# Performance work log

Measured on AMD Instinct MI355X. Metric: run time of the kernel, lower is better.

Reference implementation:

```python
import jax, jax.numpy as jnp
import numpy as np

N_NODES = 50000
N_EDGES = 600000
F_IN = 57
HID = 128
NEG_SLOPE = 0.2  # PyG GATConv default leaky_relu slope


def setup_inputs() -> dict:
    key = jax.random.key(0)
    ks = jax.random.split(key, 10)
    s = lambda k, shape, fan: jax.random.normal(k, shape, jnp.float32) / np.float32(np.sqrt(fan))
    x = jax.random.normal(ks[0], (N_NODES, F_IN), jnp.float32)
    edge_index = jax.random.randint(ks[1], (2, N_EDGES), 0, N_NODES)
    return {
        "x": x,
        "edge_index": edge_index,
        # layer1: GATConv(57 -> 128, heads=1)
        "W_gat": s(ks[2], (F_IN, HID), F_IN),
        "a_src": s(ks[3], (HID,), HID),
        "a_dst": s(ks[4], (HID,), HID),
        "b_gat": jnp.zeros((HID,), jnp.float32),
        # layer2: SAGEConv(128 -> 128, aggr='mean'): lin_l (with bias) on aggregated, lin_r (no bias) on self
        "W_l": s(ks[5], (HID, HID), HID),
        "b_l": jnp.zeros((HID,), jnp.float32),
        "W_r": s(ks[6], (HID, HID), HID),
        # layer3: Linear(128 -> 1)
        "W_out": s(ks[7], (HID, 1), HID),
        "b_out": jnp.zeros((1,), jnp.float32),
    }


def _gat_conv(x, src, dst, W, a_s, a_d, b, n):
    # PyG GATConv (heads=1): adds self-loops, attention softmax over incoming edges per dst node.
    loop = jnp.arange(n)
    src = jnp.concatenate([src, loop])
    dst = jnp.concatenate([dst, loop])
    h = x @ W                                   # [N, H]
    logit = jax.nn.leaky_relu((h @ a_s)[src] + (h @ a_d)[dst], NEG_SLOPE)  # [E+N]
    lmax = jax.lax.stop_gradient(jax.ops.segment_max(logit, dst, num_segments=n))
    ex = jnp.exp(logit - lmax[dst])
    denom = jax.ops.segment_sum(ex, dst, num_segments=n)
    alpha = ex / denom[dst]
    out = jax.ops.segment_sum(alpha[:, None] * h[src], dst, num_segments=n)  # [N, H]
    return out + b


def _sage_conv_mean(x, src, dst, W_l, b_l, W_r, n):
    # PyG SAGEConv: out = lin_l(mean_{j->i} x_j) + lin_r(x_i); no self-loops.
    msum = jax.ops.segment_sum(x[src], dst, num_segments=n)          # [N, H]
    cnt = jax.ops.segment_sum(jnp.ones_like(src, jnp.float32), dst, num_segments=n)
    mean = msum / jnp.maximum(cnt, 1.0)[:, None]
    return mean @ W_l + b_l + x @ W_r


def reference(x, edge_index, W_gat, a_src, a_dst, b_gat, W_l, b_l, W_r, W_out, b_out):
    n = x.shape[0]
    src, dst = edge_index[0], edge_index[1]
    h = jax.nn.relu(_gat_conv(x, src, dst, W_gat, a_src, a_dst, b_gat, n))
    h = jax.nn.relu(_sage_conv_mean(h, src, dst, W_l, b_l, W_r, n))
    return jax.nn.sigmoid(h @ W_out + b_out)  # [N, 1]
```

## Files before the change

kernel.cpp:

```cpp
#include <hip/hip_runtime.h>

#define NN 50000
#define NE 600000
#define F_IN 57
#define HID 128
#define NEG 0.2f
#define NB_SCAN ((NN + 255) / 256)

#define GIN_NODES 64
#define NB_GIN ((NN + GIN_NODES - 1) / GIN_NODES)
#define XST 68

#define DN_NODES 64
#define NB_DENSE ((NN + DN_NODES - 1) / DN_NODES)

typedef unsigned short bf16_t;
typedef __attribute__((ext_vector_type(8))) short bf16x8;
typedef __attribute__((ext_vector_type(4))) float f32x4;

__device__ __forceinline__ float leaky(float v) { return v >= 0.f ? v : NEG * v; }
__device__ __forceinline__ float bf2f(bf16_t u) { return __uint_as_float(((unsigned)u) << 16); }
__device__ __forceinline__ bf16_t f2bf(float f) {
    unsigned u = __float_as_uint(f);
    return (bf16_t)((u + 0x7FFFu + ((u >> 16) & 1u)) >> 16);
}

__global__ __launch_bounds__(256) void k_gat_in(
    const float* __restrict__ x, const float* __restrict__ Wg,
    const float* __restrict__ a_s, const float* __restrict__ a_d,
    bf16_t* __restrict__ h, float* __restrict__ hs, float* __restrict__ hd) {
    __shared__ float WgS[F_IN * HID];
    __shared__ float xsT[F_IN][XST];
    int tid = threadIdx.x;
    int node0 = blockIdx.x * GIN_NODES;
    {
        const float4* g = (const float4*)Wg;
        float4* s = (float4*)WgS;
        for (int i = tid; i < F_IN * HID / 4; i += 256) s[i] = g[i];
    }
    for (int i = tid; i < GIN_NODES * F_IN; i += 256) {
        int n = i / F_IN;
        int k = i - n * F_IN;
        int gn = node0 + n;
        if (gn >= NN) gn = NN - 1;
        xsT[k][n] = x[gn * F_IN + k];
    }
    __syncthreads();

    int fq = tid & 31, nq = tid >> 5;
    int f0 = fq * 4, nb = nq * 8;
    float acc[8][4];
#pragma unroll
    for (int i = 0; i < 8; ++i)
#pragma unroll
        for (int j = 0; j < 4; ++j) acc[i][j] = 0.f;

    for (int k = 0; k < F_IN; ++k) {
        float4 w = *(const float4*)&WgS[k * HID + f0];
        float4 xa = *(const float4*)&xsT[k][nb];
        float4 xb = *(const float4*)&xsT[k][nb + 4];
        float xv[8] = {xa.x, xa.y, xa.z, xa.w, xb.x, xb.y, xb.z, xb.w};
        float wv[4] = {w.x, w.y, w.z, w.w};
#pragma unroll
        for (int i = 0; i < 8; ++i)
#pragma unroll
            for (int j = 0; j < 4; ++j)
                acc[i][j] = fmaf(xv[i], wv[j], acc[i][j]);
    }

    float4 as4 = *(const float4*)(a_s + f0);
    float4 ad4 = *(const float4*)(a_d + f0);
    float ps[8], pd[8];
#pragma unroll
    for (int i = 0; i < 8; ++i) {
        int gn = node0 + nb + i;
        if (gn < NN) {
            ushort4 hv;
            hv.x = f2bf(acc[i][0]); hv.y = f2bf(acc[i][1]);
            hv.z = f2bf(acc[i][2]); hv.w = f2bf(acc[i][3]);
            *(ushort4*)(h + (size_t)gn * HID + f0) = hv;
        }
        ps[i] = acc[i][0] * as4.x + acc[i][1] * as4.y + acc[i][2] * as4.z + acc[i][3] * as4.w;
        pd[i] = acc[i][0] * ad4.x + acc[i][1] * ad4.y + acc[i][2] * ad4.z + acc[i][3] * ad4.w;
    }
#pragma unroll
    for (int off = 16; off > 0; off >>= 1) {
#pragma unroll
        for (int i = 0; i < 8; ++i) {
            ps[i] += __shfl_xor(ps[i], off);
            pd[i] += __shfl_xor(pd[i], off);
        }
    }
    if (fq == 0) {
#pragma unroll
        for (int i = 0; i < 8; ++i) {
            int gn = node0 + nb + i;
            if (gn < NN) { hs[gn] = ps[i]; hd[gn] = pd[i]; }
        }
    }
}

__global__ __launch_bounds__(256) void k_pack_w(
    const float* __restrict__ Wl, const float* __restrict__ Wr, bf16_t* __restrict__ Bp) {
    int idx = blockIdx.x * 256 + threadIdx.x;
    if (idx >= 8 * 8 * 64) return;
    int lane = idx & 63;
    int kb = (idx >> 6) & 7;
    int nt = idx >> 9;
    int col = nt * 16 + (lane & 15);
    int kbase = kb * 32 + (lane >> 4) * 8;
    bf16_t v[8];
#pragma unroll
    for (int j = 0; j < 8; ++j) {
        int k = kbase + j;
        float w = (k < HID) ? Wl[k * HID + col] : Wr[(k - HID) * HID + col];
        v[j] = f2bf(w);
    }
    ushort4* o = (ushort4*)(Bp + (size_t)idx * 8);
    ushort4 lo, hi;
    lo.x = v[0]; lo.y = v[1]; lo.z = v[2]; lo.w = v[3];
    hi.x = v[4]; hi.y = v[5]; hi.z = v[6]; hi.w = v[7];
    o[0] = lo; o[1] = hi;
}

__global__ void k_hist(const int* __restrict__ dst, int* __restrict__ deg) {
    int e = blockIdx.x * blockDim.x + threadIdx.x;
    if (e < NE) atomicAdd(&deg[dst[e]], 1);
}

__global__ void k_scan1(const int* __restrict__ deg, int* __restrict__ rptr, int* __restrict__ bsum) {
    int t = threadIdx.x;
    int i = blockIdx.x * 256 + t;
    int v = (i < NN) ? deg[i] : 0;
    __shared__ int s[256];
    s[t] = v;
    __syncthreads();
    for (int off = 1; off < 256; off <<= 1) {
        int x = (t >= off) ? s[t - off] : 0;
        __syncthreads();
        s[t] += x;
        __syncthreads();
    }
    if (i < NN) rptr[i] = s[t] - v;
    if (t == 255) bsum[blockIdx.x] = s[255];
}

__global__ void k_scan3(int* __restrict__ rptr, const int* __restrict__ bsum) {
    int t = threadIdx.x;
    int v = (t < NB_SCAN && t < blockIdx.x) ? bsum[t] : 0;
#pragma unroll
    for (int off = 32; off > 0; off >>= 1) v += __shfl_xor(v, off);
    __shared__ int wsum[4];
    if ((t & 63) == 0) wsum[t >> 6] = v;
    __syncthreads();
    int pre = wsum[0] + wsum[1] + wsum[2] + wsum[3];
    int i = blockIdx.x * 256 + t;
    if (i < NN) rptr[i] += pre;
}

__global__ void k_fill(const int* __restrict__ src, const int* __restrict__ dst,
                       const int* __restrict__ rptr, int* __restrict__ fill,
                       int* __restrict__ esrc) {
    int e = blockIdx.x * blockDim.x + threadIdx.x;
    if (e >= NE) return;
    int d = dst[e];
    int pos = rptr[d] + atomicAdd(&fill[d], 1);
    esrc[pos] = src[e];
}

__global__ __launch_bounds__(256) void k_gat_agg(
    const int* __restrict__ rptr, const int* __restrict__ deg,
    const int* __restrict__ esrc, const float* __restrict__ hs,
    const float* __restrict__ hd, const bf16_t* __restrict__ h,
    const float* __restrict__ bg, bf16_t* __restrict__ h1) {
    int tid = threadIdx.x;
    int row = blockIdx.x * 4 + (tid >> 6);
    if (row >= NN) return;
    int lane = tid & 63;
    int slot = lane >> 4;
    int f8 = lane & 15;

    int start = rptr[row];
    int dn = deg[row];
    int end = start + dn;
    float hdr = hd[row];
    float wself = __expf(leaky(hs[row] + hdr));

    float a[8];
#pragma unroll
    for (int j = 0; j < 8; ++j) a[j] = 0.f;
    float denL = 0.f;

    if (slot == 0) {
        bf16x8 r = *(const bf16x8*)(h + (size_t)row * HID + f8 * 8);
#pragma unroll
        for (int j = 0; j < 8; ++j) a[j] = wself * bf2f((bf16_t)r[j]);
    }

    int e = start;
    for (; e + 8 <= end; e += 8) {
        int s0 = esrc[e + slot];
        int s1 = esrc[e + 4 + slot];
        float w0 = __expf(leaky(hs[s0] + hdr));
        float w1 = __expf(leaky(hs[s1] + hdr));
        bf16x8 r0 = *(const bf16x8*)(h + (size_t)s0 * HID + f8 * 8);
        bf16x8 r1 = *(const bf16x8*)(h + (size_t)s1 * HID + f8 * 8);
        denL += w0 + w1;
#pragma unroll
        for (int j = 0; j < 8; ++j) {
            a[j] = fmaf(w0, bf2f((bf16_t)r0[j]), a[j]);
            a[j] = fmaf(w1, bf2f((bf16_t)r1[j]), a[j]);
        }
    }
    for (; e < end; e += 4) {
        int i = e + slot;
        bool act = i < end;
        int sn = esrc[act ? i : end - 1];
        float w = act ? __expf(leaky(hs[sn] + hdr)) : 0.f;
        bf16x8 r = *(const bf16x8*)(h + (size_t)sn * HID + f8 * 8);
        denL += w;
#pragma unroll
        for (int j = 0; j < 8; ++j) a[j] = fmaf(w, bf2f((bf16_t)r[j]), a[j]);
    }

#pragma unroll
    for (int j = 0; j < 8; ++j) {
        a[j] += __shfl_xor(a[j], 16);
        a[j] += __shfl_xor(a[j], 32);
    }
    denL += __shfl_xor(denL, 16);
    denL += __shfl_xor(denL, 32);
    float inv = 1.f / (wself + denL);

    if (lane < 16) {
        float4 b0 = *(const float4*)(bg + lane * 8);
        float4 b1 = *(const float4*)(bg + lane * 8 + 4);
        float bb[8] = {b0.x, b0.y, b0.z, b0.w, b1.x, b1.y, b1.z, b1.w};
        bf16x8 o;
#pragma unroll
        for (int j = 0; j < 8; ++j) {
            float v = a[j] * inv + bb[j];
            o[j] = (short)f2bf(v > 0.f ? v : 0.f);
        }
        *(bf16x8*)(h1 + (size_t)row * HID + lane * 8) = o;
    }
}

__global__ __launch_bounds__(256) void k_sage_gather(
    const int* __restrict__ rptr, const int* __restrict__ deg,
    const int* __restrict__ esrc, const bf16_t* __restrict__ h1,
    bf16_t* __restrict__ mean) {
    int tid = threadIdx.x;
    int row = blockIdx.x * 4 + (tid >> 6);
    if (row >= NN) return;
    int lane = tid & 63;
    int slot = lane >> 4;
    int f8 = lane & 15;

    int start = rptr[row];
    int dn = deg[row];
    int end = start + dn;

    float a[8];
#pragma unroll
    for (int j = 0; j < 8; ++j) a[j] = 0.f;

    int e = start;
    for (; e + 8 <= end; e += 8) {
        int s0 = esrc[e + slot];
        int s1 = esrc[e + 4 + slot];
        bf16x8 r0 = *(const bf16x8*)(h1 + (size_t)s0 * HID + f8 * 8);
        bf16x8 r1 = *(const bf16x8*)(h1 + (size_t)s1 * HID + f8 * 8);
#pragma unroll
        for (int j = 0; j < 8; ++j)
            a[j] += bf2f((bf16_t)r0[j]) + bf2f((bf16_t)r1[j]);
    }
    for (; e < end; e += 4) {
        int i = e + slot;
        bool act = i < end;
        int sn = esrc[act ? i : end - 1];
        bf16x8 r = *(const bf16x8*)(h1 + (size_t)sn * HID + f8 * 8);
        float w = act ? 1.f : 0.f;
#pragma unroll
        for (int j = 0; j < 8; ++j) a[j] = fmaf(w, bf2f((bf16_t)r[j]), a[j]);
    }

#pragma unroll
    for (int j = 0; j < 8; ++j) {
        a[j] += __shfl_xor(a[j], 16);
        a[j] += __shfl_xor(a[j], 32);
    }
    if (lane < 16) {
        float inv = 1.f / (float)(dn > 0 ? dn : 1);
        bf16x8 o;
#pragma unroll
        for (int j = 0; j < 8; ++j) o[j] = (short)f2bf(a[j] * inv);
        *(bf16x8*)(mean + (size_t)row * HID + lane * 8) = o;
    }
}

__global__ __launch_bounds__(256) void k_dense_mfma(
    const bf16_t* __restrict__ mean, const bf16_t* __restrict__ h1,
    const bf16_t* __restrict__ Bp, const float* __restrict__ bl,
    const float* __restrict__ Wout, const float* __restrict__ bout,
    float* __restrict__ out) {
    int tid = threadIdx.x;
    int lane = tid & 63;
    int wv = tid >> 6;
    int node0 = blockIdx.x * DN_NODES + wv * 16;
    int arow = lane & 15;
    int kg = lane >> 4;
    int gn = node0 + arow;
    if (gn >= NN) gn = NN - 1;
    const bf16_t* mrow = mean + (size_t)gn * HID;
    const bf16_t* srow = h1 + (size_t)gn * HID;
    const bf16x8* bp = (const bf16x8*)Bp;

    f32x4 acc[8];
#pragma unroll
    for (int n = 0; n < 8; ++n) acc[n] = (f32x4){0.f, 0.f, 0.f, 0.f};

#pragma unroll
    for (int kb = 0; kb < 8; ++kb) {
        int k0 = kb * 32 + kg * 8;
        bf16x8 a = (kb < 4) ? *(const bf16x8*)(mrow + k0)
                            : *(const bf16x8*)(srow + (k0 - HID));
#pragma unroll
        for (int n = 0; n < 8; ++n) {
            bf16x8 b = bp[((n * 8 + kb) << 6) + lane];
            acc[n] = __builtin_amdgcn_mfma_f32_16x16x32_bf16(a, b, acc[n], 0, 0, 0);
        }
    }

    float pr[4] = {0.f, 0.f, 0.f, 0.f};
#pragma unroll
    for (int n = 0; n < 8; ++n) {
        int f = n * 16 + arow;
        float b = bl[f];
        float wo = Wout[f];
#pragma unroll
        for (int r = 0; r < 4; ++r) {
            float v = fmaxf(acc[n][r] + b, 0.f);
            pr[r] = fmaf(v, wo, pr[r]);
        }
    }
#pragma unroll
    for (int off = 8; off > 0; off >>= 1) {
#pragma unroll
        for (int r = 0; r < 4; ++r) pr[r] += __shfl_xor(pr[r], off);
    }
    if (arow == 0) {
        float bo = bout[0];
#pragma unroll
        for (int r = 0; r < 4; ++r) {
            int gno = node0 + kg * 4 + r;
            if (gno < NN) out[gno] = 1.f / (1.f + __expf(-(pr[r] + bo)));
        }
    }
}

extern "C" void kernel_launch(void* const* d_in, const int* in_sizes, int n_in,
                              void* d_out, int out_size, void* d_ws, size_t ws_size,
                              hipStream_t stream) {
    const float* x    = (const float*)d_in[0];
    const int*   ei   = (const int*)d_in[1];
    const float* Wg   = (const float*)d_in[2];
    const float* a_s  = (const float*)d_in[3];
    const float* a_d  = (const float*)d_in[4];
    const float* bg   = (const float*)d_in[5];
    const float* Wl   = (const float*)d_in[6];
    const float* bl   = (const float*)d_in[7];
    const float* Wr   = (const float*)d_in[8];
    const float* Wout = (const float*)d_in[9];
    const float* bout = (const float*)d_in[10];
    float* out = (float*)d_out;

    const int* src = ei;
    const int* dst = ei + NE;

    bf16_t* h    = (bf16_t*)d_ws;
    bf16_t* h1   = h + (size_t)NN * HID;
    bf16_t* mean = h1 + (size_t)NN * HID;
    bf16_t* Bp   = mean + (size_t)NN * HID;
    float* hs = (float*)(Bp + 8 * 8 * 64 * 8);
    float* hd = hs + NN;
    int* deg  = (int*)(hd + NN);
    int* fill = deg + NN;
    int* rptr = fill + NN;
    int* bsum = rptr + NN;
    int* esrc = bsum + NB_SCAN;

    hipMemsetAsync(deg, 0, (size_t)2 * NN * sizeof(int), stream);

    k_pack_w<<<16, 256, 0, stream>>>(Wl, Wr, Bp);
    k_gat_in<<<NB_GIN, 256, 0, stream>>>(x, Wg, a_s, a_d, h, hs, hd);

    k_hist<<<(NE + 255) / 256, 256, 0, stream>>>(dst, deg);
    k_scan1<<<NB_SCAN, 256, 0, stream>>>(deg, rptr, bsum);
    k_scan3<<<NB_SCAN, 256, 0, stream>>>(rptr, bsum);
    k_fill<<<(NE + 255) / 256, 256, 0, stream>>>(src, dst, rptr, fill, esrc);

    k_gat_agg<<<(NN + 3) / 4, 256, 0, stream>>>(rptr, deg, esrc, hs, hd, h, bg, h1);
    k_sage_gather<<<(NN + 3) / 4, 256, 0, stream>>>(rptr, deg, esrc, h1, mean);
    k_dense_mfma<<<NB_DENSE, 256, 0, stream>>>(mean, h1, Bp, bl, Wout, bout, out);
}
```

Before: 170.7 us.

## Merge front kernels and memset, fold scan into single-pass last-block scan

```diff
diff --git a/kernel.cpp b/kernel.cpp
--- a/kernel.cpp
+++ b/kernel.cpp
@@ -10,6 +10,9 @@
 #define GIN_NODES 64
 #define NB_GIN ((NN + GIN_NODES - 1) / GIN_NODES)
 #define XST 68
+#define NB_PACK 16
+#define NZERO_INT4 ((2 * NN + 4 + 3) / 4)
+#define NB_ZERO ((NZERO_INT4 + 255) / 256)
 
 #define DN_NODES 64
 #define NB_DENSE ((NN + DN_NODES - 1) / DN_NODES)
@@ -25,13 +28,44 @@
     return (bf16_t)((u + 0x7FFFu + ((u >> 16) & 1u)) >> 16);
 }
 
-__global__ __launch_bounds__(256) void k_gat_in(
+__global__ __launch_bounds__(256) void k_front(
     const float* __restrict__ x, const float* __restrict__ Wg,
     const float* __restrict__ a_s, const float* __restrict__ a_d,
-    bf16_t* __restrict__ h, float* __restrict__ hs, float* __restrict__ hd) {
+    const float* __restrict__ Wl, const float* __restrict__ Wr,
+    bf16_t* __restrict__ h, float* __restrict__ hs, float* __restrict__ hd,
+    bf16_t* __restrict__ Bp, int* __restrict__ zbase) {
+    int tid = threadIdx.x;
+
+    if (blockIdx.x >= NB_GIN + NB_PACK) {
+        int idx4 = (blockIdx.x - NB_GIN - NB_PACK) * 256 + tid;
+        if (idx4 < NZERO_INT4) *(int4*)(zbase + idx4 * 4) = (int4){0, 0, 0, 0};
+        return;
+    }
+    if (blockIdx.x >= NB_GIN) {
+        int idx = (blockIdx.x - NB_GIN) * 256 + tid;
+        if (idx >= 8 * 8 * 64) return;
+        int lane = idx & 63;
+        int kb = (idx >> 6) & 7;
+        int nt = idx >> 9;
+        int col = nt * 16 + (lane & 15);
+        int kbase = kb * 32 + (lane >> 4) * 8;
+        bf16_t v[8];
+#pragma unroll
+        for (int j = 0; j < 8; ++j) {
+            int k = kbase + j;
+            float w = (k < HID) ? Wl[k * HID + col] : Wr[(k - HID) * HID + col];
+            v[j] = f2bf(w);
+        }
+        ushort4* o = (ushort4*)(Bp + (size_t)idx * 8);
+        ushort4 lo, hi;
+        lo.x = v[0]; lo.y = v[1]; lo.z = v[2]; lo.w = v[3];
+        hi.x = v[4]; hi.y = v[5]; hi.z = v[6]; hi.w = v[7];
+        o[0] = lo; o[1] = hi;
+        return;
+    }
+
     __shared__ float WgS[F_IN * HID];
     __shared__ float xsT[F_IN][XST];
-    int tid = threadIdx.x;
     int node0 = blockIdx.x * GIN_NODES;
     {
         const float4* g = (const float4*)Wg;
@@ -100,79 +134,63 @@
     }
 }
 
-__global__ __launch_bounds__(256) void k_pack_w(
-    const float* __restrict__ Wl, const float* __restrict__ Wr, bf16_t* __restrict__ Bp) {
-    int idx = blockIdx.x * 256 + threadIdx.x;
-    if (idx >= 8 * 8 * 64) return;
-    int lane = idx & 63;
-    int kb = (idx >> 6) & 7;
-    int nt = idx >> 9;
-    int col = nt * 16 + (lane & 15);
-    int kbase = kb * 32 + (lane >> 4) * 8;
-    bf16_t v[8];
-#pragma unroll
-    for (int j = 0; j < 8; ++j) {
-        int k = kbase + j;
-        float w = (k < HID) ? Wl[k * HID + col] : Wr[(k - HID) * HID + col];
-        v[j] = f2bf(w);
-    }
-    ushort4* o = (ushort4*)(Bp + (size_t)idx * 8);
-    ushort4 lo, hi;
-    lo.x = v[0]; lo.y = v[1]; lo.z = v[2]; lo.w = v[3];
-    hi.x = v[4]; hi.y = v[5]; hi.z = v[6]; hi.w = v[7];
-    o[0] = lo; o[1] = hi;
-}
-
 __global__ void k_hist(const int* __restrict__ dst, int* __restrict__ deg) {
     int e = blockIdx.x * blockDim.x + threadIdx.x;
     if (e < NE) atomicAdd(&deg[dst[e]], 1);
 }
 
-__global__ void k_scan1(const int* __restrict__ deg, int* __restrict__ rptr, int* __restrict__ bsum) {
+__global__ void k_scan(const int* __restrict__ deg, int* __restrict__ rptr,
+                       int* __restrict__ bsum, int* __restrict__ bpre,
+                       int* __restrict__ done) {
     int t = threadIdx.x;
-    int i = blockIdx.x * 256 + t;
+    int tile = blockIdx.x;
+    int i = tile * 256 + t;
     int v = (i < NN) ? deg[i] : 0;
     __shared__ int s[256];
+    __shared__ int islast;
     s[t] = v;
     __syncthreads();
     for (int off = 1; off < 256; off <<= 1) {
-        int x = (t >= off) ? s[t - off] : 0;
+        int xv = (t >= off) ? s[t - off] : 0;
         __syncthreads();
-        s[t] += x;
+        s[t] += xv;
         __syncthreads();
     }
     if (i < NN) rptr[i] = s[t] - v;
-    if (t == 255) bsum[blockIdx.x] = s[255];
-}
-
-__global__ void k_scan3(int* __restrict__ rptr, const int* __restrict__ bsum) {
-    int t = threadIdx.x;
-    int v = (t < NB_SCAN && t < blockIdx.x) ? bsum[t] : 0;
-#pragma unroll
-    for (int off = 32; off > 0; off >>= 1) v += __shfl_xor(v, off);
-    __shared__ int wsum[4];
-    if ((t & 63) == 0) wsum[t >> 6] = v;
+    if (t == 255) bsum[tile] = s[255];
+    __threadfence();
+    if (t == 0) islast = (atomicAdd(done, 1) == NB_SCAN - 1);
     __syncthreads();
-    int pre = wsum[0] + wsum[1] + wsum[2] + wsum[3];
-    int i = blockIdx.x * 256 + t;
-    if (i < NN) rptr[i] += pre;
+    if (!islast) return;
+    int b = (t < NB_SCAN) ? atomicAdd(&bsum[t], 0) : 0;
+    __syncthreads();
+    s[t] = b;
+    __syncthreads();
+    for (int off = 1; off < 256; off <<= 1) {
+        int xv = (t >= off) ? s[t - off] : 0;
+        __syncthreads();
+        s[t] += xv;
+        __syncthreads();
+    }
+    if (t < NB_SCAN) bpre[t] = s[t] - b;
 }
 
 __global__ void k_fill(const int* __restrict__ src, const int* __restrict__ dst,
-                       const int* __restrict__ rptr, int* __restrict__ fill,
-                       int* __restrict__ esrc) {
+                       const int* __restrict__ rptr, const int* __restrict__ bpre,
+                       int* __restrict__ fillcnt, int* __restrict__ esrc) {
     int e = blockIdx.x * blockDim.x + threadIdx.x;
     if (e >= NE) return;
     int d = dst[e];
-    int pos = rptr[d] + atomicAdd(&fill[d], 1);
+    int pos = rptr[d] + bpre[d >> 8] + atomicAdd(&fillcnt[d], 1);
     esrc[pos] = src[e];
 }
 
 __global__ __launch_bounds__(256) void k_gat_agg(
-    const int* __restrict__ rptr, const int* __restrict__ deg,
-    const int* __restrict__ esrc, const float* __restrict__ hs,
-    const float* __restrict__ hd, const bf16_t* __restrict__ h,
-    const float* __restrict__ bg, bf16_t* __restrict__ h1) {
+    const int* __restrict__ rptr, const int* __restrict__ bpre,
+    const int* __restrict__ deg, const int* __restrict__ esrc,
+    const float* __restrict__ hs, const float* __restrict__ hd,
+    const bf16_t* __restrict__ h, const float* __restrict__ bg,
+    bf16_t* __restrict__ h1) {
     int tid = threadIdx.x;
     int row = blockIdx.x * 4 + (tid >> 6);
     if (row >= NN) return;
@@ -180,7 +198,7 @@
     int slot = lane >> 4;
     int f8 = lane & 15;
 
-    int start = rptr[row];
+    int start = rptr[row] + bpre[row >> 8];
     int dn = deg[row];
     int end = start + dn;
     float hdr = hd[row];
@@ -247,9 +265,9 @@
 }
 
 __global__ __launch_bounds__(256) void k_sage_gather(
-    const int* __restrict__ rptr, const int* __restrict__ deg,
-    const int* __restrict__ esrc, const bf16_t* __restrict__ h1,
-    bf16_t* __restrict__ mean) {
+    const int* __restrict__ rptr, const int* __restrict__ bpre,
+    const int* __restrict__ deg, const int* __restrict__ esrc,
+    const bf16_t* __restrict__ h1, bf16_t* __restrict__ mean) {
     int tid = threadIdx.x;
     int row = blockIdx.x * 4 + (tid >> 6);
     if (row >= NN) return;
@@ -257,7 +275,7 @@
     int slot = lane >> 4;
     int f8 = lane & 15;
 
-    int start = rptr[row];
+    int start = rptr[row] + bpre[row >> 8];
     int dn = deg[row];
     int end = start + dn;
 
@@ -384,23 +402,22 @@
     bf16_t* Bp   = mean + (size_t)NN * HID;
     float* hs = (float*)(Bp + 8 * 8 * 64 * 8);
     float* hd = hs + NN;
-    int* deg  = (int*)(hd + NN);
-    int* fill = deg + NN;
-    int* rptr = fill + NN;
-    int* bsum = rptr + NN;
-    int* esrc = bsum + NB_SCAN;
-
-    hipMemsetAsync(deg, 0, (size_t)2 * NN * sizeof(int), stream);
-
-    k_pack_w<<<16, 256, 0, stream>>>(Wl, Wr, Bp);
-    k_gat_in<<<NB_GIN, 256, 0, stream>>>(x, Wg, a_s, a_d, h, hs, hd);
+    int* deg     = (int*)(hd + NN);
+    int* fillcnt = deg + NN;
+    int* done    = fillcnt + NN;
+    int* rptr    = done + 4;
+    int* bsum    = rptr + NN;
+    int* bpre    = bsum + 256;
+    int* esrc    = bpre + 256;
+
+    k_front<<<NB_GIN + NB_PACK + NB_ZERO, 256, 0, stream>>>(
+        x, Wg, a_s, a_d, Wl, Wr, h, hs, hd, Bp, deg);
 
     k_hist<<<(NE + 255) / 256, 256, 0, stream>>>(dst, deg);
-    k_scan1<<<NB_SCAN, 256, 0, stream>>>(deg, rptr, bsum);
-    k_scan3<<<NB_SCAN, 256, 0, stream>>>(rptr, bsum);
-    k_fill<<<(NE + 255) / 256, 256, 0, stream>>>(src, dst, rptr, fill, esrc);
-
-    k_gat_agg<<<(NN + 3) / 4, 256, 0, stream>>>(rptr, deg, esrc, hs, hd, h, bg, h1);
-    k_sage_gather<<<(NN + 3) / 4, 256, 0, stream>>>(rptr, deg, esrc, h1, mean);
+    k_scan<<<NB_SCAN, 256, 0, stream>>>(deg, rptr, bsum, bpre, done);
+    k_fill<<<(NE + 255) / 256, 256, 0, stream>>>(src, dst, rptr, bpre, fillcnt, esrc);
+
+    k_gat_agg<<<(NN + 3) / 4, 256, 0, stream>>>(rptr, bpre, deg, esrc, hs, hd, h, bg, h1);
+    k_sage_gather<<<(NN + 3) / 4, 256, 0, stream>>>(rptr, bpre, deg, esrc, h1, mean);
     k_dense_mfma<<<NB_DENSE, 256, 0, stream>>>(mean, h1, Bp, bl, Wout, bout, out);
 }
```

After: 175.0 us. 2.5% more time.
